# Performance work log

Measured on AMD Instinct MI355X. Metric: run time of the kernel, lower is better.

## Reference

```python
import jax, jax.numpy as jnp
import numpy as np

B, T, F, D, H, L, DFF, G = 4, 2048, 512, 1024, 16, 2, 4096, 16
WSCALE = 0.03  # ~1/sqrt(D) so activations stay well-conditioned


def setup_inputs() -> dict:
    key = jax.random.key(0)
    ks = iter(jax.random.split(key, 24))

    def w(shape):
        return jax.random.normal(next(ks), shape, jnp.float32) * WSCALE

    return {
        "x": jax.random.normal(next(ks), (B, T, F), jnp.float32),
        "proj_w": w((D, F)), "proj_b": jnp.zeros((D,), jnp.float32),
        "wq": w((L, D, D)), "wk": w((L, D, D)), "wv": w((L, D, D)),
        "bq": jnp.zeros((L, D), jnp.float32), "bk": jnp.zeros((L, D), jnp.float32), "bv": jnp.zeros((L, D), jnp.float32),
        "wo": w((L, D, D)), "bo": jnp.zeros((L, D), jnp.float32),
        "ln1_g": jnp.ones((L, D), jnp.float32), "ln1_b": jnp.zeros((L, D), jnp.float32),
        "ln2_g": jnp.ones((L, D), jnp.float32), "ln2_b": jnp.zeros((L, D), jnp.float32),
        "w1": w((L, DFF, D)), "b1": jnp.zeros((L, DFF), jnp.float32),
        "w2": w((L, D, DFF)), "b2": jnp.zeros((L, D), jnp.float32),
        "hw1": w((G, D, D)), "hb1": jnp.zeros((G, D), jnp.float32),
        "hw2": w((G, 2, D)), "hb2": jnp.zeros((G, 2), jnp.float32),
        "nhead": H,
    }


def _ln(x, g, b, eps=1e-5):
    m = x.mean(-1, keepdims=True)
    v = ((x - m) ** 2).mean(-1, keepdims=True)
    return (x - m) * jax.lax.rsqrt(v + eps) * g + b


def _pe(t, d):
    # sinusoidal positional encoding, shape (t, d) (d even -> sin/cos interleave)
    pos = jnp.arange(t, dtype=jnp.float32)[:, None]
    div = jnp.exp(jnp.arange(0, d, 2, dtype=jnp.float32) * (-np.log(10000.0) / d))
    ph = pos * div
    return jnp.stack([jnp.sin(ph), jnp.cos(ph)], axis=-1).reshape(t, d)


def reference(x, proj_w, proj_b, wq, wk, wv, bq, bk, bv, wo, bo,
              ln1_g, ln1_b, ln2_g, ln2_b, w1, b1, w2, b2,
              hw1, hb1, hw2, hb2, nhead):
    Bx, Tx, _ = x.shape
    Dm = proj_w.shape[0]
    dh = Dm // nhead
    h = x @ proj_w.T + proj_b + _pe(Tx, Dm)  # (B,T,D)
    for l in range(wq.shape[0]):  # post-norm encoder layers
        q = (h @ wq[l].T + bq[l]).reshape(Bx, Tx, nhead, dh)
        k = (h @ wk[l].T + bk[l]).reshape(Bx, Tx, nhead, dh)
        v = (h @ wv[l].T + bv[l]).reshape(Bx, Tx, nhead, dh)
        # explicit (non-fused) attention path, as forced by need_weights=True
        scores = jnp.einsum('bthd,bshd->bhts', q, k) / jnp.sqrt(jnp.float32(dh))
        attn = jax.nn.softmax(scores, axis=-1)  # (B,H,T,T)
        ctx = jnp.einsum('bhts,bshd->bthd', attn, v).reshape(Bx, Tx, Dm)
        h = _ln(h + ctx @ wo[l].T + bo[l], ln1_g[l], ln1_b[l])
        ff = jax.nn.relu(h @ w1[l].T + b1[l]) @ w2[l].T + b2[l]
        h = _ln(h + ff, ln2_g[l], ln2_b[l])
    hl = h[:, -1, :]  # last-token pooling, (B,D)
    z = jax.nn.relu(jnp.einsum('bd,gkd->bgk', hl, hw1) + hb1)  # per-sector hidden
    logits = jnp.einsum('bgk,gok->bgo', z, hw2) + hb2           # (B,G,2)
    return jax.nn.softmax(logits, axis=-1)
```

## Files before the change

kernel.cpp:

```cpp
#include <hip/hip_runtime.h>
#include <hip/hip_bf16.h>
#include <cstdint>
#include <cstddef>


typedef __bf16 bf16_t;
typedef __attribute__((ext_vector_type(8))) __bf16 bf16x8;
typedef __attribute__((ext_vector_type(4))) __bf16 bf16x4;
typedef __attribute__((ext_vector_type(4))) float f32x4;

#define DEV __device__ __forceinline__
#define AS1 __attribute__((address_space(1)))
#define AS3 __attribute__((address_space(3)))

DEV void gload_lds16(const void* g, void* l) {
  __builtin_amdgcn_global_load_lds((AS1 void*)(g), (AS3 void*)(l), 16, 0, 0);
}

DEV char* swz_ptr(void* base, int row, int colb) {
  return (char*)base + row * 128 + ((((colb >> 4) ^ (row & 7))) << 4) + (colb & 15);
}
DEV const char* swz_ptr(const void* base, int row, int colb) {
  return (const char*)base + row * 128 + ((((colb >> 4) ^ (row & 7))) << 4) +
         (colb & 15);
}

__global__ __launch_bounds__(256) void f2b_kernel(const float* __restrict__ s,
                                                  bf16_t* __restrict__ d, int n4) {
  const int i = blockIdx.x * 256 + threadIdx.x;
  if (i >= n4) return;
  const float4 v = *(const float4*)&s[(size_t)i * 4];
  bf16x4 o = {(bf16_t)v.x, (bf16_t)v.y, (bf16_t)v.z, (bf16_t)v.w};
  *(bf16x4*)&d[(size_t)i * 4] = o;
}

__global__ __launch_bounds__(256) void bcat_kernel(const float* __restrict__ bq,
                                                   const float* __restrict__ bk,
                                                   const float* __restrict__ bv,
                                                   float* __restrict__ out) {
  const int idx = blockIdx.x * 256 + threadIdx.x;
  const int l = idx / 3072, r = idx - l * 3072;
  const int p = r >> 10, i = r & 1023;
  const float* s = (p == 0) ? bq : ((p == 1) ? bk : bv);
  out[idx] = s[l * 1024 + i];
}

__global__ __launch_bounds__(256) void pe_kernel(float* __restrict__ pe) {
  const int idx = blockIdx.x * 256 + threadIdx.x;
  const int t = idx >> 9, i = idx & 511;
  const float dv = __expf((float)(2 * i) * -0.008994473019508785f);
  const float ph = (float)t * dv;
  pe[(size_t)t * 1024 + 2 * i] = sinf(ph);
  pe[(size_t)t * 1024 + 2 * i + 1] = cosf(ph);
}

template <int EPI, int BN>
__global__ __launch_bounds__(512, 2) void gemm9(
    const bf16_t* __restrict__ A, const bf16_t* __restrict__ W,
    const float* __restrict__ bias, bf16_t* __restrict__ outb,
    float* __restrict__ outf, const float* __restrict__ res32,
    const float* __restrict__ pe, int M, int N, int K) {
  constexpr int NBB = BN / 64;
  constexpr int LPT = 4 + NBB;
  constexpr int MF = (BN == 256) ? 8 : 4;
  constexpr int BUFSZ = 32768 + BN * 128;
  __shared__ char smem[2][BUFSZ];
  const int tid = threadIdx.x, wv = tid >> 6, ln = tid & 63;
  const int nwg = gridDim.x * gridDim.y;
  int bid = blockIdx.y * gridDim.x + blockIdx.x;
  bid = (bid & 7) * (nwg >> 3) + (bid >> 3);
  const int m0 = (bid / gridDim.x) * 256, n0 = (bid % gridDim.x) * BN;
  const int wrow = (BN == 256) ? (wv >> 2) * 128 : (wv >> 1) * 64;
  const int wcol = (BN == 256) ? (wv & 3) * 64 : (wv & 1) * 64;
  f32x4 acc[MF][4] = {};

  const int tp = tid ^ ((tid >> 3) & 7);
  const int srow = tp >> 3, sc8 = (tp & 7) * 8;
  const bf16_t* pa[4];
  const bf16_t* pb[NBB];
#pragma unroll
  for (int u = 0; u < 4; ++u) pa[u] = A + (size_t)(m0 + u * 64 + srow) * K + sc8;
#pragma unroll
  for (int u = 0; u < NBB; ++u) pb[u] = W + (size_t)(n0 + u * 64 + srow) * K + sc8;
  const int wvb = wv * 1024;

  auto stage = [&](int s) {
    char* bA = &smem[s][0] + wvb;
    char* bB = &smem[s][32768] + wvb;
#pragma unroll
    for (int u = 0; u < 4; ++u) {
      gload_lds16(pa[u], bA + u * 8192);
      pa[u] += 64;
    }
#pragma unroll
    for (int u = 0; u < NBB; ++u) {
      gload_lds16(pb[u], bB + u * 8192);
      pb[u] += 64;
    }
  };

  auto wait_lpt = [&]() {
    if constexpr (LPT == 8)
      asm volatile("s_waitcnt vmcnt(8)" ::: "memory");
    else
      asm volatile("s_waitcnt vmcnt(6)" ::: "memory");
  };

  const int NK = K >> 6;
  stage(0);
  stage(1);
  wait_lpt();
  __builtin_amdgcn_s_barrier();

  for (int kt = 0; kt < NK; ++kt) {
    const char* bA = &smem[kt & 1][0];
    const char* bB = &smem[kt & 1][32768];
#pragma unroll
    for (int ks = 0; ks < 2; ++ks) {
      const int cb = ks * 64 + (ln >> 4) * 16;
      bf16x8 bF[4];
#pragma unroll
      for (int n = 0; n < 4; ++n) {
        const int lb = (wcol + n * 16 + (ln & 15)) * 128 + cb;
        bF[n] = *(const bf16x8*)(bB + (lb ^ (((lb >> 7) & 7) << 4)));
      }
#pragma unroll
      for (int mh = 0; mh < 2; ++mh) {
        bf16x8 aF[MF / 2];
#pragma unroll
        for (int m = 0; m < MF / 2; ++m) {
          const int lb = (wrow + (mh * (MF / 2) + m) * 16 + (ln & 15)) * 128 + cb;
          aF[m] = *(const bf16x8*)(bA + (lb ^ (((lb >> 7) & 7) << 4)));
        }
        __builtin_amdgcn_s_setprio(1);
#pragma unroll
        for (int m = 0; m < MF / 2; ++m)
#pragma unroll
          for (int n = 0; n < 4; ++n)
            acc[mh * (MF / 2) + m][n] = __builtin_amdgcn_mfma_f32_16x16x32_bf16(
                aF[m], bF[n], acc[mh * (MF / 2) + m][n], 0, 0, 0);
        __builtin_amdgcn_s_setprio(0);
      }
    }
    __builtin_amdgcn_s_barrier();
    if (kt + 2 < NK) {
      stage(kt & 1);
      wait_lpt();
    } else if (kt + 1 < NK) {
      asm volatile("s_waitcnt vmcnt(0)" ::: "memory");
    }
    __builtin_amdgcn_s_barrier();
    __builtin_amdgcn_sched_barrier(0);
  }

  const int rr = (ln >> 4) * 4, cc = ln & 15;
#pragma unroll
  for (int m = 0; m < MF; ++m) {
    const int rowb = m0 + wrow + m * 16 + rr;
#pragma unroll
    for (int n = 0; n < 4; ++n) {
      const int col = n0 + wcol + n * 16 + cc;
      const float bv = bias[col];
#pragma unroll
      for (int r = 0; r < 4; ++r) {
        const int row = rowb + r;
        float v = acc[m][n][r] + bv;
        const size_t o = (size_t)row * N + col;
        if constexpr (EPI == 1) {
          v = fmaxf(v, 0.f);
          outb[o] = (bf16_t)v;
        } else if constexpr (EPI == 2) {
          v += pe[(size_t)(row & 2047) * 1024 + col];
          outb[o] = (bf16_t)v;
          outf[o] = v;
        } else if constexpr (EPI == 3) {
          v += res32[o];
          outf[o] = v;
        } else {
          outb[o] = (bf16_t)v;
        }
      }
    }
  }
}

__global__ __launch_bounds__(256) void ln_kernel(const float* __restrict__ pre,
                                                 const float* __restrict__ g,
                                                 const float* __restrict__ b,
                                                 bf16_t* __restrict__ h16,
                                                 float* __restrict__ h32) {
  const int row = blockIdx.x, tid = threadIdx.x;
  const size_t base = (size_t)row * 1024 + tid * 4;
  const float4 v = *(const float4*)&pre[base];
  float s = v.x + v.y + v.z + v.w;
  float s2 = v.x * v.x + v.y * v.y + v.z * v.z + v.w * v.w;
#pragma unroll
  for (int m = 1; m < 64; m <<= 1) {
    s += __shfl_xor(s, m);
    s2 += __shfl_xor(s2, m);
  }
  __shared__ float ls[4], ls2[4];
  if ((tid & 63) == 0) {
    ls[tid >> 6] = s;
    ls2[tid >> 6] = s2;
  }
  __syncthreads();
  s = ls[0] + ls[1] + ls[2] + ls[3];
  s2 = ls2[0] + ls2[1] + ls2[2] + ls2[3];
  const float mean = s * (1.f / 1024.f);
  const float var = s2 * (1.f / 1024.f) - mean * mean;
  const float rs = rsqrtf(var + 1e-5f);
  const float4 gv = *(const float4*)&g[tid * 4];
  const float4 bv = *(const float4*)&b[tid * 4];
  const float o0 = (v.x - mean) * rs * gv.x + bv.x;
  const float o1 = (v.y - mean) * rs * gv.y + bv.y;
  const float o2 = (v.z - mean) * rs * gv.z + bv.z;
  const float o3 = (v.w - mean) * rs * gv.w + bv.w;
  bf16x4 ob = {(bf16_t)o0, (bf16_t)o1, (bf16_t)o2, (bf16_t)o3};
  *(bf16x4*)&h16[base] = ob;
  float4 of = {o0, o1, o2, o3};
  *(float4*)&h32[base] = of;
}

__global__ __launch_bounds__(256) void transpose_v(const bf16_t* __restrict__ v,
                                                   bf16_t* __restrict__ vt) {
  __shared__ bf16_t tile[64][80];
  const int bh = blockIdx.y, t0 = blockIdx.x * 64;
  const int tid = threadIdx.x;
  const int b = bh >> 4;
  const size_t vbase = ((size_t)(b * 2048 + t0)) * 3072 + (bh & 15) * 64;
#pragma unroll
  for (int p = 0; p < 2; ++p) {
    const int chunk = p * 256 + tid;
    const int tr = chunk >> 3, c8 = (chunk & 7) * 8;
    *(bf16x8*)&tile[tr][c8] = *(const bf16x8*)&v[vbase + (size_t)tr * 3072 + c8];
  }
  __syncthreads();
  const int d = tid >> 2, t8 = (tid & 3) * 16;
  bf16_t tmp[16];
#pragma unroll
  for (int j = 0; j < 16; ++j) tmp[j] = tile[t8 + j][d];
  const size_t obase = ((size_t)bh * 64 + d) * 2048 + t0 + t8;
  *(bf16x8*)&vt[obase] = *(bf16x8*)&tmp[0];
  *(bf16x8*)&vt[obase + 8] = *(bf16x8*)&tmp[8];
}

__global__ __launch_bounds__(256, 4) void attn_kernel(const bf16_t* __restrict__ qkv,
                                                      const bf16_t* __restrict__ vt,
                                                      bf16_t* __restrict__ ctx) {
  constexpr float SCL = 0.18033688011112042f;
  constexpr int QS = 3072;
  __shared__ bf16_t lK[2][64 * 64];
  __shared__ bf16_t lV[2][64 * 64];
  __shared__ bf16_t lP[4][16 * 64];
  const int tid = threadIdx.x, wv = tid >> 6, ln = tid & 63;
  const int nwg = gridDim.x * gridDim.y;
  int bid = blockIdx.y * gridDim.x + blockIdx.x;
  bid = (bid & 7) * (nwg >> 3) + (bid >> 3);
  const int bh = bid / gridDim.x, b = bh >> 4, h = bh & 15;
  const int q0 = (bid % gridDim.x) * 64;
  const int qrow = q0 + wv * 16 + (ln & 15);
  const bf16_t* qp = qkv + (size_t)(b * 2048 + qrow) * QS + h * 64 + (ln >> 4) * 8;
  const bf16x8 aQ0 = *(const bf16x8*)qp;
  const bf16x8 aQ1 = *(const bf16x8*)(qp + 32);
  f32x4 O[4] = {};
  float m_q = -1e30f, l_q = 0.f;
  const int sr = tid >> 3;
  const int scS = ((tid & 7) ^ ((tid >> 3) & 7)) * 8;
  const bf16_t* kp0 = qkv + 1024 + (size_t)(b * 2048 + sr) * QS + h * 64 + scS;
  const bf16_t* kp1 = kp0 + (size_t)32 * QS;
  const bf16_t* vp0 = vt + (size_t)bh * 64 * 2048 + (size_t)sr * 2048 + scS;
  const bf16_t* vp1 = vp0 + 32 * 2048;

  auto stage = [&](int bufi) {
    char* dk = (char*)&lK[bufi][0] + wv * 1024;
    char* dv = (char*)&lV[bufi][0] + wv * 1024;
    gload_lds16(kp0, dk);
    gload_lds16(kp1, dk + 4096);
    gload_lds16(vp0, dv);
    gload_lds16(vp1, dv + 4096);
    kp0 += (size_t)64 * QS;
    kp1 += (size_t)64 * QS;
    vp0 += 64;
    vp1 += 64;
  };

  stage(0);
  asm volatile("s_waitcnt vmcnt(0)" ::: "memory");
  __builtin_amdgcn_s_barrier();

  for (int st = 0; st < 32; ++st) {
    const int cur = st & 1;
    if (st + 1 < 32) stage(cur ^ 1);
    f32x4 sc[4] = {};
    __builtin_amdgcn_s_setprio(1);
#pragma unroll
    for (int ks = 0; ks < 2; ++ks) {
      const int ko = ks * 32 + (ln >> 4) * 8;
      const bf16x8 aQ = ks ? aQ1 : aQ0;
#pragma unroll
      for (int nt = 0; nt < 4; ++nt) {
        const bf16x8 bK = *(const bf16x8*)swz_ptr(&lK[cur][0], nt * 16 + (ln & 15), ko * 2);
        sc[nt] = __builtin_amdgcn_mfma_f32_16x16x32_bf16(bK, aQ, sc[nt], 0, 0, 0);
      }
    }
    __builtin_amdgcn_s_setprio(0);
    float mx = fmaxf(fmaxf(sc[0][0], sc[0][1]), fmaxf(sc[0][2], sc[0][3]));
#pragma unroll
    for (int nt = 1; nt < 4; ++nt)
      mx = fmaxf(mx, fmaxf(fmaxf(sc[nt][0], sc[nt][1]), fmaxf(sc[nt][2], sc[nt][3])));
    mx *= SCL;
    mx = fmaxf(mx, __shfl_xor(mx, 16));
    mx = fmaxf(mx, __shfl_xor(mx, 32));
    if (__any(mx > m_q + 8.f)) {
      const float mnew = fmaxf(m_q, mx);
      const float alpha = exp2f(m_q - mnew);
      m_q = mnew;
      l_q *= alpha;
      float ar[4];
#pragma unroll
      for (int r = 0; r < 4; ++r) ar[r] = __shfl(alpha, (ln >> 4) * 4 + r);
#pragma unroll
      for (int dt = 0; dt < 4; ++dt)
#pragma unroll
        for (int r = 0; r < 4; ++r) O[dt][r] *= ar[r];
    }
    float rs = 0.f;
#pragma unroll
    for (int nt = 0; nt < 4; ++nt) {
      bf16x4 pb;
#pragma unroll
      for (int r = 0; r < 4; ++r) {
        const float p = exp2f(sc[nt][r] * SCL - m_q);
        rs += p;
        pb[r] = (bf16_t)p;
      }
      *(bf16x4*)swz_ptr(&lP[wv][0], ln & 15, nt * 32 + (ln >> 4) * 8) = pb;
    }
    rs += __shfl_xor(rs, 16);
    rs += __shfl_xor(rs, 32);
    l_q += rs;
    __builtin_amdgcn_s_setprio(1);
#pragma unroll
    for (int ks = 0; ks < 2; ++ks) {
      const int ko = ks * 32 + (ln >> 4) * 8;
      const bf16x8 aP = *(const bf16x8*)swz_ptr(&lP[wv][0], ln & 15, ko * 2);
#pragma unroll
      for (int dt = 0; dt < 4; ++dt) {
        const bf16x8 bV = *(const bf16x8*)swz_ptr(&lV[cur][0], dt * 16 + (ln & 15), ko * 2);
        O[dt] = __builtin_amdgcn_mfma_f32_16x16x32_bf16(aP, bV, O[dt], 0, 0, 0);
      }
    }
    __builtin_amdgcn_s_setprio(0);
    asm volatile("s_waitcnt vmcnt(0)" ::: "memory");
    __builtin_amdgcn_s_barrier();
    __builtin_amdgcn_sched_barrier(0);
  }
  const float invl = 1.f / l_q;
  float ir[4];
#pragma unroll
  for (int r = 0; r < 4; ++r) ir[r] = __shfl(invl, (ln >> 4) * 4 + r);
  const int orow = b * 2048 + q0 + wv * 16 + (ln >> 4) * 4;
#pragma unroll
  for (int r = 0; r < 4; ++r) {
#pragma unroll
    for (int dt = 0; dt < 4; ++dt)
      ctx[((size_t)(orow + r)) * 1024 + h * 64 + dt * 16 + (ln & 15)] =
          (bf16_t)(O[dt][r] * ir[r]);
  }
}

__global__ __launch_bounds__(256) void head_z(const float* __restrict__ h32,
                                              const float* __restrict__ hw1,
                                              const float* __restrict__ hb1,
                                              float* __restrict__ z) {
  const int g = blockIdx.x, slab = blockIdx.y;
  const int wv = threadIdx.x >> 6, ln = threadIdx.x & 63;
  float4 hl[4][4];
#pragma unroll
  for (int b = 0; b < 4; ++b)
#pragma unroll
    for (int c = 0; c < 4; ++c)
      hl[b][c] = *(const float4*)&h32[((size_t)b * 2048 + 2047) * 1024 + c * 256 + ln * 4];
  const int k0 = slab * 64 + wv * 16;
  for (int kk = 0; kk < 16; ++kk) {
    const int kq = k0 + kk;
    const float* wrow = hw1 + ((size_t)g * 1024 + kq) * 1024;
    float p[4] = {0, 0, 0, 0};
#pragma unroll
    for (int c = 0; c < 4; ++c) {
      const float4 w4 = *(const float4*)&wrow[c * 256 + ln * 4];
#pragma unroll
      for (int b = 0; b < 4; ++b)
        p[b] += w4.x * hl[b][c].x + w4.y * hl[b][c].y + w4.z * hl[b][c].z +
                w4.w * hl[b][c].w;
    }
#pragma unroll
    for (int m = 1; m < 64; m <<= 1)
#pragma unroll
      for (int b = 0; b < 4; ++b) p[b] += __shfl_xor(p[b], m);
    if (ln == 0) {
#pragma unroll
      for (int b = 0; b < 4; ++b)
        z[((size_t)b * 16 + g) * 1024 + kq] = fmaxf(p[b] + hb1[g * 1024 + kq], 0.f);
    }
  }
}

__global__ __launch_bounds__(64) void head_logits(const float* __restrict__ z,
                                                  const float* __restrict__ hw2,
                                                  const float* __restrict__ hb2,
                                                  float* __restrict__ out) {
  const int b = blockIdx.x, g = blockIdx.y, ln = threadIdx.x;
  const float* zr = z + ((size_t)b * 16 + g) * 1024;
  const float* w0 = hw2 + (size_t)g * 2048;
  const float* w1 = w0 + 1024;
  float p0 = 0.f, p1 = 0.f;
#pragma unroll
  for (int c = 0; c < 4; ++c) {
    const float4 zv = *(const float4*)&zr[c * 256 + ln * 4];
    const float4 a0 = *(const float4*)&w0[c * 256 + ln * 4];
    const float4 a1 = *(const float4*)&w1[c * 256 + ln * 4];
    p0 += zv.x * a0.x + zv.y * a0.y + zv.z * a0.z + zv.w * a0.w;
    p1 += zv.x * a1.x + zv.y * a1.y + zv.z * a1.z + zv.w * a1.w;
  }
#pragma unroll
  for (int m = 1; m < 64; m <<= 1) {
    p0 += __shfl_xor(p0, m);
    p1 += __shfl_xor(p1, m);
  }
  if (ln == 0) {
    const float l0 = p0 + hb2[g * 2], l1 = p1 + hb2[g * 2 + 1];
    const float mx = fmaxf(l0, l1);
    const float e0 = expf(l0 - mx), e1 = expf(l1 - mx);
    const float inv = 1.f / (e0 + e1);
    out[(size_t)b * 32 + g * 2] = e0 * inv;
    out[(size_t)b * 32 + g * 2 + 1] = e1 * inv;
  }
}

extern "C" void kernel_launch(void* const* d_in, const int* in_sizes, int n_in,
                              void* d_out, int out_size, void* d_ws, size_t ws_size,
                              hipStream_t stream) {
  const float* x = (const float*)d_in[0];
  const float* proj_w = (const float*)d_in[1];
  const float* proj_b = (const float*)d_in[2];
  const float* wq = (const float*)d_in[3];
  const float* wk = (const float*)d_in[4];
  const float* wvv = (const float*)d_in[5];
  const float* bq = (const float*)d_in[6];
  const float* bk = (const float*)d_in[7];
  const float* bv = (const float*)d_in[8];
  const float* wo = (const float*)d_in[9];
  const float* bo = (const float*)d_in[10];
  const float* ln1_g = (const float*)d_in[11];
  const float* ln1_b = (const float*)d_in[12];
  const float* ln2_g = (const float*)d_in[13];
  const float* ln2_b = (const float*)d_in[14];
  const float* w1 = (const float*)d_in[15];
  const float* b1 = (const float*)d_in[16];
  const float* w2 = (const float*)d_in[17];
  const float* b2 = (const float*)d_in[18];
  const float* hw1 = (const float*)d_in[19];
  const float* hb1 = (const float*)d_in[20];
  const float* hw2 = (const float*)d_in[21];
  const float* hb2 = (const float*)d_in[22];
  float* out = (float*)d_out;
  char* ws = (char*)d_ws;

  size_t o = 0;
  auto take = [&](size_t bytes) { size_t r = o; o += bytes; return r; };
  const size_t o_wqkv = take(12582912);
  const size_t o_wo = take(4194304);
  const size_t o_w1 = take(16777216);
  const size_t o_w2 = take(16777216);
  const size_t o_pw = take(1048576);
  const size_t o_h16 = take(16777216);
  const size_t o_h32 = take(33554432);
  const size_t o_pre = take(33554432);
  const size_t o_r4 = take(67108864);
  const size_t o_r5 = take(16777216);
  const size_t o_z = take(262144);
  const size_t o_bqkv = take(24576);

  bf16_t* wqkv16 = (bf16_t*)(ws + o_wqkv);
  bf16_t* wo16 = (bf16_t*)(ws + o_wo);
  bf16_t* w1_16 = (bf16_t*)(ws + o_w1);
  bf16_t* w2_16 = (bf16_t*)(ws + o_w2);
  bf16_t* pw16 = (bf16_t*)(ws + o_pw);
  bf16_t* h16 = (bf16_t*)(ws + o_h16);
  float* h32 = (float*)(ws + o_h32);
  float* pre32 = (float*)(ws + o_pre);
  bf16_t* qkv16 = (bf16_t*)(ws + o_r4);
  bf16_t* vT16 = (bf16_t*)(ws + o_r4 + 50331648);
  bf16_t* ff1 = (bf16_t*)(ws + o_r4);
  bf16_t* x16 = (bf16_t*)(ws + o_r5);
  float* pe32 = (float*)(ws + o_r5 + 8388608);
  bf16_t* ctx16 = (bf16_t*)(ws + o_r5);
  float* zbuf = (float*)(ws + o_z);
  float* bqkv = (float*)(ws + o_bqkv);

  f2b_kernel<<<4096, 256, 0, stream>>>(x, x16, 1048576);
  f2b_kernel<<<512, 256, 0, stream>>>(proj_w, pw16, 131072);
  for (int l = 0; l < 2; ++l) {
    f2b_kernel<<<1024, 256, 0, stream>>>(wq + (size_t)l * 1048576,
                                         wqkv16 + (size_t)(l * 3 + 0) * 1048576, 262144);
    f2b_kernel<<<1024, 256, 0, stream>>>(wk + (size_t)l * 1048576,
                                         wqkv16 + (size_t)(l * 3 + 1) * 1048576, 262144);
    f2b_kernel<<<1024, 256, 0, stream>>>(wvv + (size_t)l * 1048576,
                                         wqkv16 + (size_t)(l * 3 + 2) * 1048576, 262144);
  }
  f2b_kernel<<<2048, 256, 0, stream>>>(wo, wo16, 524288);
  f2b_kernel<<<8192, 256, 0, stream>>>(w1, w1_16, 2097152);
  f2b_kernel<<<8192, 256, 0, stream>>>(w2, w2_16, 2097152);
  bcat_kernel<<<24, 256, 0, stream>>>(bq, bk, bv, bqkv);
  pe_kernel<<<4096, 256, 0, stream>>>(pe32);

  gemm9<2, 128><<<dim3(8, 32), 512, 0, stream>>>(x16, pw16, proj_b, h16, h32, nullptr,
                                                 pe32, 8192, 1024, 512);

  for (int l = 0; l < 2; ++l) {
    const bf16_t* wqkv_l = wqkv16 + (size_t)l * 3145728;
    const bf16_t* wo_l = wo16 + (size_t)l * 1048576;
    const bf16_t* w1_l = w1_16 + (size_t)l * 4194304;
    const bf16_t* w2_l = w2_16 + (size_t)l * 4194304;

    gemm9<0, 256><<<dim3(12, 32), 512, 0, stream>>>(h16, wqkv_l, bqkv + l * 3072, qkv16,
                                                    nullptr, nullptr, nullptr, 8192,
                                                    3072, 1024);
    transpose_v<<<dim3(32, 64), 256, 0, stream>>>(qkv16 + 2048, vT16);
    attn_kernel<<<dim3(32, 64), 256, 0, stream>>>(qkv16, vT16, ctx16);
    gemm9<3, 128><<<dim3(8, 32), 512, 0, stream>>>(ctx16, wo_l, bo + l * 1024, nullptr,
                                                   pre32, h32, nullptr, 8192, 1024,
                                                   1024);
    ln_kernel<<<8192, 256, 0, stream>>>(pre32, ln1_g + l * 1024, ln1_b + l * 1024, h16,
                                        h32);
    gemm9<1, 256><<<dim3(16, 32), 512, 0, stream>>>(h16, w1_l, b1 + l * 4096, ff1,
                                                    nullptr, nullptr, nullptr, 8192,
                                                    4096, 1024);
    gemm9<3, 128><<<dim3(8, 32), 512, 0, stream>>>(ff1, w2_l, b2 + l * 1024, nullptr,
                                                   pre32, h32, nullptr, 8192, 1024,
                                                   4096);
    ln_kernel<<<8192, 256, 0, stream>>>(pre32, ln2_g + l * 1024, ln2_b + l * 1024, h16,
                                        h32);
  }

  head_z<<<dim3(16, 16), 256, 0, stream>>>(h32, hw1, hb1, zbuf);
  head_logits<<<dim3(4, 16), 64, 0, stream>>>(zbuf, hw2, hb2, out);
}
```

Before: 954.2 us.

## Rewrite attention with 32x32 MFMA register-resident P; add 128x128 GEMM tiles

The attention kernel moves from 16x16x32 to 32x32x16 MFMA, and each wave now handles 32 query rows, so a block covers 128 queries and the grid is halved. The softmax probabilities are packed to bf16 in registers and rearranged with permlane32 swaps instead of going through an LDS round-trip, which removes the lP buffer. The GEMM template gains a BM parameter so the N=1024 GEMMs run with 128x128 tiles on 256 threads, doubling the grid for better CU fill. This raises register pressure in attention (occupancy hint drops from 4 to 3) and uses smaller GEMM tiles with less reuse per block.

```diff
diff --git a/kernel.cpp b/kernel.cpp
--- a/kernel.cpp
+++ b/kernel.cpp
@@ -8,6 +8,9 @@
 typedef __attribute__((ext_vector_type(8))) __bf16 bf16x8;
 typedef __attribute__((ext_vector_type(4))) __bf16 bf16x4;
 typedef __attribute__((ext_vector_type(4))) float f32x4;
+typedef __attribute__((ext_vector_type(16))) float f32x16;
+typedef __attribute__((ext_vector_type(2))) unsigned u32x2;
+typedef __attribute__((ext_vector_type(4))) unsigned u32x4;
 
 #define DEV __device__ __forceinline__
 #define AS1 __attribute__((address_space(1)))
@@ -17,12 +20,24 @@
   __builtin_amdgcn_global_load_lds((AS1 void*)(g), (AS3 void*)(l), 16, 0, 0);
 }
 
-DEV char* swz_ptr(void* base, int row, int colb) {
-  return (char*)base + row * 128 + ((((colb >> 4) ^ (row & 7))) << 4) + (colb & 15);
-}
 DEV const char* swz_ptr(const void* base, int row, int colb) {
   return (const char*)base + row * 128 + ((((colb >> 4) ^ (row & 7))) << 4) +
          (colb & 15);
+}
+
+DEV unsigned cvtpk(float lo, float hi) {
+  unsigned r;
+  asm("v_cvt_pk_bf16_f32 %0, %1, %2" : "=v"(r) : "v"(lo), "v"(hi));
+  return r;
+}
+DEV void swap32(unsigned& a, unsigned& b) {
+  u32x2 r = __builtin_amdgcn_permlane32_swap(a, b, false, false);
+  a = r[0];
+  b = r[1];
+}
+DEV bf16x8 mkfrag(unsigned w0, unsigned w1, unsigned w2, unsigned w3) {
+  u32x4 v = {w0, w1, w2, w3};
+  return __builtin_bit_cast(bf16x8, v);
 }
 
 __global__ __launch_bounds__(256) void f2b_kernel(const float* __restrict__ s,
@@ -54,47 +69,51 @@
   pe[(size_t)t * 1024 + 2 * i + 1] = cosf(ph);
 }
 
-template <int EPI, int BN>
-__global__ __launch_bounds__(512, 2) void gemm9(
+template <int EPI, int BM, int BN>
+__global__ __launch_bounds__(BM == 256 ? 512 : 256, 2) void gemm9(
     const bf16_t* __restrict__ A, const bf16_t* __restrict__ W,
     const float* __restrict__ bias, bf16_t* __restrict__ outb,
     float* __restrict__ outf, const float* __restrict__ res32,
     const float* __restrict__ pe, int M, int N, int K) {
-  constexpr int NBB = BN / 64;
-  constexpr int LPT = 4 + NBB;
-  constexpr int MF = (BN == 256) ? 8 : 4;
-  constexpr int BUFSZ = 32768 + BN * 128;
+  constexpr int T = (BM == 256) ? 512 : 256;
+  constexpr int RPC = T / 8;
+  constexpr int NA = (BM * 128) / (T * 16);
+  constexpr int NB = (BN * 128) / (T * 16);
+  constexpr int LPT = NA + NB;
+  constexpr int MF = (BM == 256) ? 8 : 4;
+  constexpr int ASZ = BM * 128;
+  constexpr int BUFSZ = (BM + BN) * 128;
   __shared__ char smem[2][BUFSZ];
   const int tid = threadIdx.x, wv = tid >> 6, ln = tid & 63;
   const int nwg = gridDim.x * gridDim.y;
   int bid = blockIdx.y * gridDim.x + blockIdx.x;
   bid = (bid & 7) * (nwg >> 3) + (bid >> 3);
-  const int m0 = (bid / gridDim.x) * 256, n0 = (bid % gridDim.x) * BN;
-  const int wrow = (BN == 256) ? (wv >> 2) * 128 : (wv >> 1) * 64;
-  const int wcol = (BN == 256) ? (wv & 3) * 64 : (wv & 1) * 64;
+  const int m0 = (bid / gridDim.x) * BM, n0 = (bid % gridDim.x) * BN;
+  const int wrow = (BM == 256) ? (wv >> 2) * 128 : (wv >> 1) * 64;
+  const int wcol = (BM == 256) ? (wv & 3) * 64 : (wv & 1) * 64;
   f32x4 acc[MF][4] = {};
 
   const int tp = tid ^ ((tid >> 3) & 7);
   const int srow = tp >> 3, sc8 = (tp & 7) * 8;
-  const bf16_t* pa[4];
-  const bf16_t* pb[NBB];
-#pragma unroll
-  for (int u = 0; u < 4; ++u) pa[u] = A + (size_t)(m0 + u * 64 + srow) * K + sc8;
-#pragma unroll
-  for (int u = 0; u < NBB; ++u) pb[u] = W + (size_t)(n0 + u * 64 + srow) * K + sc8;
+  const bf16_t* pa[NA];
+  const bf16_t* pb[NB];
+#pragma unroll
+  for (int u = 0; u < NA; ++u) pa[u] = A + (size_t)(m0 + u * RPC + srow) * K + sc8;
+#pragma unroll
+  for (int u = 0; u < NB; ++u) pb[u] = W + (size_t)(n0 + u * RPC + srow) * K + sc8;
   const int wvb = wv * 1024;
 
   auto stage = [&](int s) {
     char* bA = &smem[s][0] + wvb;
-    char* bB = &smem[s][32768] + wvb;
-#pragma unroll
-    for (int u = 0; u < 4; ++u) {
-      gload_lds16(pa[u], bA + u * 8192);
+    char* bB = &smem[s][ASZ] + wvb;
+#pragma unroll
+    for (int u = 0; u < NA; ++u) {
+      gload_lds16(pa[u], bA + u * (T * 16));
       pa[u] += 64;
     }
 #pragma unroll
-    for (int u = 0; u < NBB; ++u) {
-      gload_lds16(pb[u], bB + u * 8192);
+    for (int u = 0; u < NB; ++u) {
+      gload_lds16(pb[u], bB + u * (T * 16));
       pb[u] += 64;
     }
   };
@@ -114,7 +133,7 @@
 
   for (int kt = 0; kt < NK; ++kt) {
     const char* bA = &smem[kt & 1][0];
-    const char* bB = &smem[kt & 1][32768];
+    const char* bB = &smem[kt & 1][ASZ];
 #pragma unroll
     for (int ks = 0; ks < 2; ++ks) {
       const int cb = ks * 64 + (ln >> 4) * 16;
@@ -245,25 +264,25 @@
   *(bf16x8*)&vt[obase + 8] = *(bf16x8*)&tmp[8];
 }
 
-__global__ __launch_bounds__(256, 4) void attn_kernel(const bf16_t* __restrict__ qkv,
+__global__ __launch_bounds__(256, 3) void attn_kernel(const bf16_t* __restrict__ qkv,
                                                       const bf16_t* __restrict__ vt,
                                                       bf16_t* __restrict__ ctx) {
   constexpr float SCL = 0.18033688011112042f;
   constexpr int QS = 3072;
   __shared__ bf16_t lK[2][64 * 64];
   __shared__ bf16_t lV[2][64 * 64];
-  __shared__ bf16_t lP[4][16 * 64];
   const int tid = threadIdx.x, wv = tid >> 6, ln = tid & 63;
   const int nwg = gridDim.x * gridDim.y;
   int bid = blockIdx.y * gridDim.x + blockIdx.x;
   bid = (bid & 7) * (nwg >> 3) + (bid >> 3);
   const int bh = bid / gridDim.x, b = bh >> 4, h = bh & 15;
-  const int q0 = (bid % gridDim.x) * 64;
-  const int qrow = q0 + wv * 16 + (ln & 15);
-  const bf16_t* qp = qkv + (size_t)(b * 2048 + qrow) * QS + h * 64 + (ln >> 4) * 8;
-  const bf16x8 aQ0 = *(const bf16x8*)qp;
-  const bf16x8 aQ1 = *(const bf16x8*)(qp + 32);
-  f32x4 O[4] = {};
+  const int q0 = (bid % gridDim.x) * 128 + wv * 32;
+  const int lq = ln & 31, hi = ln >> 5;
+  const bf16_t* qp = qkv + (size_t)(b * 2048 + q0 + lq) * QS + h * 64 + hi * 8;
+  bf16x8 qF[4];
+#pragma unroll
+  for (int kk = 0; kk < 4; ++kk) qF[kk] = *(const bf16x8*)(qp + kk * 16);
+  f32x16 O0 = {}, O1 = {};
   float m_q = -1e30f, l_q = 0.f;
   const int sr = tid >> 3;
   const int scS = ((tid & 7) ^ ((tid >> 3) & 7)) * 8;
@@ -292,64 +311,104 @@
   for (int st = 0; st < 32; ++st) {
     const int cur = st & 1;
     if (st + 1 < 32) stage(cur ^ 1);
-    f32x4 sc[4] = {};
+    f32x16 s0 = {}, s1 = {};
     __builtin_amdgcn_s_setprio(1);
 #pragma unroll
-    for (int ks = 0; ks < 2; ++ks) {
-      const int ko = ks * 32 + (ln >> 4) * 8;
-      const bf16x8 aQ = ks ? aQ1 : aQ0;
-#pragma unroll
-      for (int nt = 0; nt < 4; ++nt) {
-        const bf16x8 bK = *(const bf16x8*)swz_ptr(&lK[cur][0], nt * 16 + (ln & 15), ko * 2);
-        sc[nt] = __builtin_amdgcn_mfma_f32_16x16x32_bf16(bK, aQ, sc[nt], 0, 0, 0);
-      }
+    for (int kk = 0; kk < 4; ++kk) {
+      const int cb = kk * 32 + hi * 16;
+      const bf16x8 k0 = *(const bf16x8*)swz_ptr(&lK[cur][0], lq, cb);
+      const bf16x8 k1 = *(const bf16x8*)swz_ptr(&lK[cur][0], 32 + lq, cb);
+      s0 = __builtin_amdgcn_mfma_f32_32x32x16_bf16(k0, qF[kk], s0, 0, 0, 0);
+      s1 = __builtin_amdgcn_mfma_f32_32x32x16_bf16(k1, qF[kk], s1, 0, 0, 0);
     }
     __builtin_amdgcn_s_setprio(0);
-    float mx = fmaxf(fmaxf(sc[0][0], sc[0][1]), fmaxf(sc[0][2], sc[0][3]));
-#pragma unroll
-    for (int nt = 1; nt < 4; ++nt)
-      mx = fmaxf(mx, fmaxf(fmaxf(sc[nt][0], sc[nt][1]), fmaxf(sc[nt][2], sc[nt][3])));
-    mx *= SCL;
-    mx = fmaxf(mx, __shfl_xor(mx, 16));
+    float t[8];
+#pragma unroll
+    for (int i = 0; i < 8; ++i)
+      t[i] = fmaxf(fmaxf(s0[2 * i], s0[2 * i + 1]),
+                   fmaxf(s1[2 * i], s1[2 * i + 1]));
+    const float u0 = fmaxf(fmaxf(t[0], t[1]), fmaxf(t[2], t[3]));
+    const float u1 = fmaxf(fmaxf(t[4], t[5]), fmaxf(t[6], t[7]));
+    float mx = fmaxf(u0, u1) * SCL;
     mx = fmaxf(mx, __shfl_xor(mx, 32));
     if (__any(mx > m_q + 8.f)) {
       const float mnew = fmaxf(m_q, mx);
       const float alpha = exp2f(m_q - mnew);
       m_q = mnew;
       l_q *= alpha;
-      float ar[4];
-#pragma unroll
-      for (int r = 0; r < 4; ++r) ar[r] = __shfl(alpha, (ln >> 4) * 4 + r);
-#pragma unroll
-      for (int dt = 0; dt < 4; ++dt)
-#pragma unroll
-        for (int r = 0; r < 4; ++r) O[dt][r] *= ar[r];
-    }
-    float rs = 0.f;
-#pragma unroll
-    for (int nt = 0; nt < 4; ++nt) {
-      bf16x4 pb;
-#pragma unroll
-      for (int r = 0; r < 4; ++r) {
-        const float p = exp2f(sc[nt][r] * SCL - m_q);
-        rs += p;
-        pb[r] = (bf16_t)p;
+#pragma unroll
+      for (int r = 0; r < 16; ++r) {
+        const float ar = __shfl(alpha, (r & 3) + 8 * (r >> 2) + 4 * hi);
+        O0[r] *= ar;
+        O1[r] *= ar;
       }
-      *(bf16x4*)swz_ptr(&lP[wv][0], ln & 15, nt * 32 + (ln >> 4) * 8) = pb;
-    }
-    rs += __shfl_xor(rs, 16);
-    rs += __shfl_xor(rs, 32);
-    l_q += rs;
+    }
+    float ra = 0.f, rb = 0.f, rc = 0.f, rd = 0.f;
+#pragma unroll
+    for (int i = 0; i < 4; ++i) {
+      s0[i] = exp2f(fmaf(s0[i], SCL, -m_q));
+      ra += s0[i];
+      s0[i + 4] = exp2f(fmaf(s0[i + 4], SCL, -m_q));
+      rb += s0[i + 4];
+      s0[i + 8] = exp2f(fmaf(s0[i + 8], SCL, -m_q));
+      rc += s0[i + 8];
+      s0[i + 12] = exp2f(fmaf(s0[i + 12], SCL, -m_q));
+      rd += s0[i + 12];
+    }
+#pragma unroll
+    for (int i = 0; i < 4; ++i) {
+      s1[i] = exp2f(fmaf(s1[i], SCL, -m_q));
+      ra += s1[i];
+      s1[i + 4] = exp2f(fmaf(s1[i + 4], SCL, -m_q));
+      rb += s1[i + 4];
+      s1[i + 8] = exp2f(fmaf(s1[i + 8], SCL, -m_q));
+      rc += s1[i + 8];
+      s1[i + 12] = exp2f(fmaf(s1[i + 12], SCL, -m_q));
+      rd += s1[i + 12];
+    }
+    float rsum = (ra + rb) + (rc + rd);
+    rsum += __shfl_xor(rsum, 32);
+    l_q += rsum;
     __builtin_amdgcn_s_setprio(1);
-#pragma unroll
-    for (int ks = 0; ks < 2; ++ks) {
-      const int ko = ks * 32 + (ln >> 4) * 8;
-      const bf16x8 aP = *(const bf16x8*)swz_ptr(&lP[wv][0], ln & 15, ko * 2);
-#pragma unroll
-      for (int dt = 0; dt < 4; ++dt) {
-        const bf16x8 bV = *(const bf16x8*)swz_ptr(&lV[cur][0], dt * 16 + (ln & 15), ko * 2);
-        O[dt] = __builtin_amdgcn_mfma_f32_16x16x32_bf16(aP, bV, O[dt], 0, 0, 0);
-      }
+    {
+      unsigned A = cvtpk(s0[0], s0[1]), Bq = cvtpk(s0[2], s0[3]);
+      unsigned C = cvtpk(s0[4], s0[5]), Dq = cvtpk(s0[6], s0[7]);
+      unsigned A2 = cvtpk(s0[8], s0[9]), B2 = cvtpk(s0[10], s0[11]);
+      unsigned C2 = cvtpk(s0[12], s0[13]), D2 = cvtpk(s0[14], s0[15]);
+      swap32(A, C);
+      swap32(Bq, Dq);
+      swap32(A2, C2);
+      swap32(B2, D2);
+      const bf16x8 f0 = mkfrag(A, Bq, C, Dq);
+      const bf16x8 f1 = mkfrag(A2, B2, C2, D2);
+      const bf16x8 v00 = *(const bf16x8*)swz_ptr(&lV[cur][0], lq, 0 + hi * 16);
+      const bf16x8 v01 = *(const bf16x8*)swz_ptr(&lV[cur][0], lq, 32 + hi * 16);
+      const bf16x8 v10 = *(const bf16x8*)swz_ptr(&lV[cur][0], 32 + lq, 0 + hi * 16);
+      const bf16x8 v11 = *(const bf16x8*)swz_ptr(&lV[cur][0], 32 + lq, 32 + hi * 16);
+      O0 = __builtin_amdgcn_mfma_f32_32x32x16_bf16(f0, v00, O0, 0, 0, 0);
+      O0 = __builtin_amdgcn_mfma_f32_32x32x16_bf16(f1, v01, O0, 0, 0, 0);
+      O1 = __builtin_amdgcn_mfma_f32_32x32x16_bf16(f0, v10, O1, 0, 0, 0);
+      O1 = __builtin_amdgcn_mfma_f32_32x32x16_bf16(f1, v11, O1, 0, 0, 0);
+    }
+    {
+      unsigned A = cvtpk(s1[0], s1[1]), Bq = cvtpk(s1[2], s1[3]);
+      unsigned C = cvtpk(s1[4], s1[5]), Dq = cvtpk(s1[6], s1[7]);
+      unsigned A2 = cvtpk(s1[8], s1[9]), B2 = cvtpk(s1[10], s1[11]);
+      unsigned C2 = cvtpk(s1[12], s1[13]), D2 = cvtpk(s1[14], s1[15]);
+      swap32(A, C);
+      swap32(Bq, Dq);
+      swap32(A2, C2);
+      swap32(B2, D2);
+      const bf16x8 f2 = mkfrag(A, Bq, C, Dq);
+      const bf16x8 f3 = mkfrag(A2, B2, C2, D2);
+      const bf16x8 v02 = *(const bf16x8*)swz_ptr(&lV[cur][0], lq, 64 + hi * 16);
+      const bf16x8 v03 = *(const bf16x8*)swz_ptr(&lV[cur][0], lq, 96 + hi * 16);
+      const bf16x8 v12 = *(const bf16x8*)swz_ptr(&lV[cur][0], 32 + lq, 64 + hi * 16);
+      const bf16x8 v13 = *(const bf16x8*)swz_ptr(&lV[cur][0], 32 + lq, 96 + hi * 16);
+      O0 = __builtin_amdgcn_mfma_f32_32x32x16_bf16(f2, v02, O0, 0, 0, 0);
+      O0 = __builtin_amdgcn_mfma_f32_32x32x16_bf16(f3, v03, O0, 0, 0, 0);
+      O1 = __builtin_amdgcn_mfma_f32_32x32x16_bf16(f2, v12, O1, 0, 0, 0);
+      O1 = __builtin_amdgcn_mfma_f32_32x32x16_bf16(f3, v13, O1, 0, 0, 0);
     }
     __builtin_amdgcn_s_setprio(0);
     asm volatile("s_waitcnt vmcnt(0)" ::: "memory");
@@ -357,16 +416,13 @@
     __builtin_amdgcn_sched_barrier(0);
   }
   const float invl = 1.f / l_q;
-  float ir[4];
-#pragma unroll
-  for (int r = 0; r < 4; ++r) ir[r] = __shfl(invl, (ln >> 4) * 4 + r);
-  const int orow = b * 2048 + q0 + wv * 16 + (ln >> 4) * 4;
-#pragma unroll
-  for (int r = 0; r < 4; ++r) {
-#pragma unroll
-    for (int dt = 0; dt < 4; ++dt)
-      ctx[((size_t)(orow + r)) * 1024 + h * 64 + dt * 16 + (ln & 15)] =
-          (bf16_t)(O[dt][r] * ir[r]);
+  const size_t obase = ((size_t)(b * 2048 + q0)) * 1024 + h * 64 + lq;
+#pragma unroll
+  for (int r = 0; r < 16; ++r) {
+    const int qr = (r & 3) + 8 * (r >> 2) + 4 * hi;
+    const float iv = __shfl(invl, qr);
+    ctx[obase + (size_t)qr * 1024] = (bf16_t)(O0[r] * iv);
+    ctx[obase + (size_t)qr * 1024 + 32] = (bf16_t)(O1[r] * iv);
   }
 }
 
@@ -516,8 +572,8 @@
   bcat_kernel<<<24, 256, 0, stream>>>(bq, bk, bv, bqkv);
   pe_kernel<<<4096, 256, 0, stream>>>(pe32);
 
-  gemm9<2, 128><<<dim3(8, 32), 512, 0, stream>>>(x16, pw16, proj_b, h16, h32, nullptr,
-                                                 pe32, 8192, 1024, 512);
+  gemm9<2, 128, 128><<<dim3(8, 64), 256, 0, stream>>>(x16, pw16, proj_b, h16, h32,
+                                                      nullptr, pe32, 8192, 1024, 512);
 
   for (int l = 0; l < 2; ++l) {
     const bf16_t* wqkv_l = wqkv16 + (size_t)l * 3145728;
@@ -525,22 +581,22 @@
     const bf16_t* w1_l = w1_16 + (size_t)l * 4194304;
     const bf16_t* w2_l = w2_16 + (size_t)l * 4194304;
 
-    gemm9<0, 256><<<dim3(12, 32), 512, 0, stream>>>(h16, wqkv_l, bqkv + l * 3072, qkv16,
-                                                    nullptr, nullptr, nullptr, 8192,
-                                                    3072, 1024);
+    gemm9<0, 256, 256><<<dim3(12, 32), 512, 0, stream>>>(h16, wqkv_l, bqkv + l * 3072,
+                                                         qkv16, nullptr, nullptr,
+                                                         nullptr, 8192, 3072, 1024);
     transpose_v<<<dim3(32, 64), 256, 0, stream>>>(qkv16 + 2048, vT16);
-    attn_kernel<<<dim3(32, 64), 256, 0, stream>>>(qkv16, vT16, ctx16);
-    gemm9<3, 128><<<dim3(8, 32), 512, 0, stream>>>(ctx16, wo_l, bo + l * 1024, nullptr,
-                                                   pre32, h32, nullptr, 8192, 1024,
-                                                   1024);
+    attn_kernel<<<dim3(16, 64), 256, 0, stream>>>(qkv16, vT16, ctx16);
+    gemm9<3, 128, 128><<<dim3(8, 64), 256, 0, stream>>>(ctx16, wo_l, bo + l * 1024,
+                                                        nullptr, pre32, h32, nullptr,
+                                                        8192, 1024, 1024);
     ln_kernel<<<8192, 256, 0, stream>>>(pre32, ln1_g + l * 1024, ln1_b + l * 1024, h16,
                                         h32);
-    gemm9<1, 256><<<dim3(16, 32), 512, 0, stream>>>(h16, w1_l, b1 + l * 4096, ff1,
-                                                    nullptr, nullptr, nullptr, 8192,
-                                                    4096, 1024);
-    gemm9<3, 128><<<dim3(8, 32), 512, 0, stream>>>(ff1, w2_l, b2 + l * 1024, nullptr,
-                                                   pre32, h32, nullptr, 8192, 1024,
-                                                   4096);
+    gemm9<1, 256, 256><<<dim3(16, 32), 512, 0, stream>>>(h16, w1_l, b1 + l * 4096, ff1,
+                                                         nullptr, nullptr, nullptr,
+                                                         8192, 4096, 1024);
+    gemm9<3, 128, 128><<<dim3(8, 64), 256, 0, stream>>>(ff1, w2_l, b2 + l * 1024,
+                                                        nullptr, pre32, h32, nullptr,
+                                                        8192, 1024, 4096);
     ln_kernel<<<8192, 256, 0, stream>>>(pre32, ln2_g + l * 1024, ln2_b + l * 1024, h16,
                                         h32);
   }
```

Result: faster. 884.7 us (-7.3%).
